# Kernel optimization log

Hardware: AMD Instinct MI355X
Metric: run time of the kernel (lower is better)

## Reference

```python
import jax, jax.numpy as jnp
import numpy as np
from jax import lax

EPS = 1e-5

def setup_inputs() -> dict:
    key = jax.random.key(0)
    ks = jax.random.split(key, 8)
    B, D, H, W = 2, 96, 96, 96
    K, N, R = 4, 16, 6
    return {
        "x": jax.random.normal(ks[0], (B, D, H, W), jnp.float32),
        "x_proj_weight": jax.random.normal(ks[1], (K, R + 2 * N, D), jnp.float32) * 0.05,
        "dt_projs_weight": jax.random.normal(ks[2], (K, D, R), jnp.float32) * 0.05,
        "dt_projs_bias": jax.random.normal(ks[3], (K, D), jnp.float32) * 0.05,
        "A_logs": jax.random.uniform(ks[4], (K * D, N), jnp.float32, 0.0, 1.0),
        "Ds": jax.random.normal(ks[5], (K * D,), jnp.float32) * 0.1,
        "norm_weight": jnp.ones((D,), jnp.float32),
        "norm_bias": jnp.zeros((D,), jnp.float32),
    }

def _cross_scan(x):
    # x: [B,C,H,W] -> xs: [B,4,C,L]; dirs: row-major, col-major, and their flips
    B, C, H, W = x.shape
    x_hw = x.reshape(B, C, H * W)
    x_wh = jnp.swapaxes(x, 2, 3).reshape(B, C, H * W)
    return jnp.stack([x_hw, x_wh, x_hw[..., ::-1], x_wh[..., ::-1]], axis=1)

def _cross_merge(ys, H, W):
    # ys: [B,4,C,L] -> y: [B,C,L]
    B, K, C, L = ys.shape
    ys = ys[:, 0:2] + ys[:, 2:4][..., ::-1]
    y_wh = jnp.swapaxes(ys[:, 1].reshape(B, C, W, H), 2, 3).reshape(B, C, L)
    return ys[:, 0] + y_wh

def _forward(x, x_proj_weight, dt_projs_weight, dt_projs_bias, A_logs, Ds,
             norm_weight, norm_bias):
    B, D, H, W = x.shape
    L = H * W
    K, _, R = dt_projs_weight.shape
    N = A_logs.shape[1]

    xs = _cross_scan(x)                                        # [B,K,D,L]
    x_dbl = jnp.einsum('bkdl,kcd->bkcl', xs, x_proj_weight)    # [B,K,R+2N,L]
    dts, Bs, Cs = x_dbl[:, :, :R], x_dbl[:, :, R:R + N], x_dbl[:, :, R + N:]
    dts = jnp.einsum('bkrl,kdr->bkdl', dts, dt_projs_weight)   # [B,K,D,L]

    A = -jnp.exp(A_logs).reshape(K, D, N)                      # [K,D,N]
    delta = jax.nn.softplus(dts + dt_projs_bias[None, :, :, None])  # [B,K,D,L]

    # time-major for scan
    u_t = jnp.moveaxis(xs, 3, 0)       # [L,B,K,D]
    d_t = jnp.moveaxis(delta, 3, 0)    # [L,B,K,D]
    B_t = jnp.moveaxis(Bs, 3, 0)       # [L,B,K,N]
    C_t = jnp.moveaxis(Cs, 3, 0)       # [L,B,K,N]

    def step(h, inp):
        u, dlt, b, c = inp
        h = jnp.exp(dlt[..., None] * A) * h + (dlt * u)[..., None] * b[:, :, None, :]
        y = jnp.einsum('bkdn,bkn->bkd', h, c)
        return h, y

    h0 = jnp.zeros((B, K, D, N), xs.dtype)
    _, ys = lax.scan(step, h0, (u_t, d_t, B_t, C_t))           # ys: [L,B,K,D]
    ys = jnp.moveaxis(ys, 0, 3)                                # [B,K,D,L]
    ys = ys + Ds.reshape(1, K, D, 1) * xs                      # skip term

    y = _cross_merge(ys, H, W)                                 # [B,D,L]
    y = jnp.swapaxes(y, 1, 2)                                  # [B,L,D]
    # out_norm: LayerNorm over channel dim
    mu = y.mean(-1, keepdims=True)
    var = y.var(-1, keepdims=True)
    y = (y - mu) / jnp.sqrt(var + EPS) * norm_weight + norm_bias
    return y.reshape(B, H, W, D)

def reference(x, x_proj_weight, dt_projs_weight, dt_projs_bias, A_logs, Ds,
              norm_weight, norm_bias):
    return _forward(x, x_proj_weight, dt_projs_weight, dt_projs_bias,
                    A_logs, Ds, norm_weight, norm_bias)
```

## Files before the change

kernel.cpp:

```cpp
#include <hip/hip_runtime.h>
#include <hip/hip_bf16.h>
#include <hip/hip_fp16.h>


constexpr int Bn = 2, Kn = 4, Dn = 96, Hn = 96, Wn = 96, Ln = Hn * Wn;
constexpr int Nn = 16, Rn = 6;
constexpr int CCn = 192, CLn = 48;

#define DI __device__ __forceinline__

DI float bf2f(unsigned short u) { return __uint_as_float(((unsigned)u) << 16); }
DI bool probe_bf16(const void* nw) { return ((const unsigned*)nw)[0] == 0x3F803F80u; }
DI float ld_in(const void* p, long i, bool bf) {
  return bf ? bf2f(((const unsigned short*)p)[i]) : ((const float*)p)[i];
}
DI float fexp2(float x) {
#if __has_builtin(__builtin_amdgcn_exp2f)
  return __builtin_amdgcn_exp2f(x);
#else
  return exp2f(x);
#endif
}
DI float softplus_fast(float v) {
  return (v > 15.f) ? v : __logf(1.f + __expf(v));
}
constexpr float LOG2E = 1.44269504088896340736f;

__global__ __launch_bounds__(256) void k_convert(
    const void* __restrict__ xpw, const void* __restrict__ dtw,
    const void* __restrict__ dtb, const void* __restrict__ Al,
    const void* __restrict__ Ds, const void* __restrict__ nw,
    const void* __restrict__ nb,
    float* __restrict__ wp_f, float* __restrict__ wdt_f,
    float* __restrict__ bias_f, float* __restrict__ Al_f,
    float* __restrict__ dsum, float* __restrict__ nw_f, float* __restrict__ nb_f) {
  bool bf = probe_bf16(nw);
  int gtid = blockIdx.x * 256 + threadIdx.x;
  int gs = gridDim.x * 256;
  for (int i = gtid; i < Kn * 38 * Dn; i += gs) wp_f[i] = ld_in(xpw, i, bf);
  for (int i = gtid; i < Kn * Dn * Rn; i += gs) wdt_f[i] = ld_in(dtw, i, bf);
  for (int i = gtid; i < Kn * Dn; i += gs) bias_f[i] = ld_in(dtb, i, bf);
  for (int i = gtid; i < Kn * Dn * Nn; i += gs)
    Al_f[i] = -__expf(ld_in(Al, i, bf)) * LOG2E;
  for (int i = gtid; i < Dn; i += gs) {
    dsum[i] = ld_in(Ds, i, bf) + ld_in(Ds, 96 + i, bf) +
              ld_in(Ds, 192 + i, bf) + ld_in(Ds, 288 + i, bf);
    nw_f[i] = ld_in(nw, i, bf);
    nb_f[i] = ld_in(nb, i, bf);
  }
}

__global__ __launch_bounds__(256) void k_prep(const void* __restrict__ x,
                                              const void* __restrict__ nwraw,
                                              float* __restrict__ xl,
                                              float* __restrict__ xlT) {
  __shared__ float tile[96 * 97];
  bool bf = probe_bf16(nwraw);
  int h = blockIdx.x, b = blockIdx.y;
  long srcbase = (long)b * Dn * Ln + (long)h * 96;
  for (int i = threadIdx.x; i < 96 * 96; i += 256) {
    int d = i / 96, w = i - d * 96;
    tile[d * 97 + w] = ld_in(x, srcbase + (long)d * Ln + w, bf);
  }
  __syncthreads();
  float* xlb = xl + (size_t)b * Ln * 96;
  float* xTb = xlT + (size_t)b * Ln * 96;
  for (int i = threadIdx.x; i < 96 * 96; i += 256) {
    int w = i / 96, d = i - w * 96;
    float v = tile[d * 97 + w];
    xlb[(size_t)(h * 96 + w) * 96 + d] = v;
    xTb[(size_t)(w * 96 + h) * 96 + d] = v;
  }
}

__global__ __launch_bounds__(256) void k_proj(
    const float* __restrict__ xl, const float* __restrict__ xlT,
    const float* __restrict__ wp_f, const float* __restrict__ wdt_f,
    const float* __restrict__ bias_f,
    __half2* __restrict__ ddu, __half* __restrict__ BCh) {
  constexpr int TL = 64;
  __shared__ __half xt[TL * 102];
  __shared__ float wp[40 * 100];
  __shared__ float xd[40 * 70];
  __shared__ float wdt[96 * 6];
  __shared__ float bias[96];
  int tile = blockIdx.x, k = blockIdx.y, b = blockIdx.z;
  int l0 = tile * TL;
  int tid = threadIdx.x;
  bool rev = (k & 2) != 0;

  for (int i = tid; i < 40 * 100; i += 256) {
    int c = i / 100, dd = i - c * 100;
    wp[i] = (c < 38 && dd < 96) ? wp_f[k * 38 * 96 + c * 96 + dd] : 0.f;
  }
  for (int i = tid; i < 96 * 6; i += 256) wdt[i] = wdt_f[k * 96 * 6 + i];
  if (tid < 96) bias[tid] = bias_f[k * 96 + tid];
  {
    const float* xsrc = ((k & 1) ? xlT : xl) + (size_t)b * Ln * 96;
    for (int i = tid; i < TL * 24; i += 256) {
      int r = i / 24, q = i - r * 24;
      int g = rev ? (Ln - 1 - l0 - r) : (l0 + r);
      float4 v = *(const float4*)(xsrc + (size_t)g * 96 + q * 4);
      *(__half2*)(&xt[r * 102 + q * 4]) = __floats2half2_rn(v.x, v.y);
      *(__half2*)(&xt[r * 102 + q * 4 + 2]) = __floats2half2_rn(v.z, v.w);
    }
  }
  __syncthreads();

  {
    int jg = tid & 31, cg = tid >> 5;
    int j0 = jg * 2, c0 = cg * 5;
    float acc[5][2];
#pragma unroll
    for (int i = 0; i < 5; ++i) { acc[i][0] = 0.f; acc[i][1] = 0.f; }
    for (int dd = 0; dd < 96; dd += 4) {
      float xv[2][4];
#pragma unroll
      for (int e = 0; e < 2; ++e) {
        float2 f01 = __half22float2(*(const __half2*)&xt[(j0 + e) * 102 + dd]);
        float2 f23 = __half22float2(*(const __half2*)&xt[(j0 + e) * 102 + dd + 2]);
        xv[e][0] = f01.x; xv[e][1] = f01.y; xv[e][2] = f23.x; xv[e][3] = f23.y;
      }
#pragma unroll
      for (int i = 0; i < 5; ++i) {
        float4 w4 = *(const float4*)(wp + (c0 + i) * 100 + dd);
        const float* w = (const float*)&w4;
#pragma unroll
        for (int q = 0; q < 4; ++q) {
          acc[i][0] = fmaf(xv[0][q], w[q], acc[i][0]);
          acc[i][1] = fmaf(xv[1][q], w[q], acc[i][1]);
        }
      }
    }
#pragma unroll
    for (int i = 0; i < 5; ++i)
      *(float2*)(xd + (c0 + i) * 70 + j0) = make_float2(acc[i][0], acc[i][1]);
  }
  __syncthreads();

  size_t bk = (size_t)b * 4 + k;
  {
    __half* o = BCh + (bk * (size_t)Ln + l0) * 32;
    for (int i = tid; i < TL * 32; i += 256) {
      int j = i >> 5, c = i & 31;
      o[i] = __float2half(xd[(6 + c) * 70 + j]);
    }
  }
  {
    int lp = tid >> 2, q = tid & 3, d0 = q * 24;
    float xr[6];
#pragma unroll
    for (int r = 0; r < 6; ++r) xr[r] = xd[r * 70 + lp];
    __half2* orow = ddu + (bk * (size_t)Ln + l0 + lp) * 96 + d0;
#pragma unroll
    for (int ii = 0; ii < 6; ++ii) {
      union { uint4 u4; __half2 h2[4]; } pk;
#pragma unroll
      for (int p = 0; p < 4; ++p) {
        int d = d0 + ii * 4 + p;
        float v = bias[d];
#pragma unroll
        for (int r = 0; r < 6; ++r) v = fmaf(xr[r], wdt[d * 6 + r], v);
        float sp = softplus_fast(v);
        float u = __half2float(xt[lp * 102 + d]);
        pk.h2[p] = __floats2half2_rn(sp, sp * u);
      }
      *(uint4*)(orow + ii * 4) = pk.u4;
    }
  }
}

__global__ __launch_bounds__(384) void k_scan1(
    const __half2* __restrict__ ddu, const __half* __restrict__ BCh,
    const float* __restrict__ Al_f, float* __restrict__ PSg) {
  __shared__ __half2 dd_s[CLn * 96];
  __shared__ __half b_s[CLn * 16];
  int chunk = blockIdx.x, k = blockIdx.y, b = blockIdx.z;
  int tid = threadIdx.x;
  int d = tid >> 2, ng = tid & 3, n0 = ng * 4;
  int bk = b * 4 + k;
  int bkd = bk * 96 + d;
  int t0 = chunk * CLn;
  float ac[4];
#pragma unroll
  for (int j = 0; j < 4; ++j) ac[j] = Al_f[(k * 96 + d) * 16 + n0 + j];
  {
    const uint4* dsrc = (const uint4*)(ddu + ((size_t)bk * Ln + t0) * 96);
    uint4* ddst = (uint4*)dd_s;
    for (int i = tid; i < CLn * 96 / 4; i += 384) ddst[i] = dsrc[i];
    const unsigned* bsrc = (const unsigned*)(BCh + ((size_t)bk * Ln + t0) * 32);
    unsigned* bdst = (unsigned*)b_s;
    for (int i = tid; i < CLn * 8; i += 384) {
      int t = i >> 3, q = i & 7;
      bdst[t * 8 + q] = bsrc[t * 16 + q];
    }
  }
  __syncthreads();

  float P[4] = {1.f, 1.f, 1.f, 1.f}, S[4] = {0.f, 0.f, 0.f, 0.f};
#pragma unroll 4
  for (int t = 0; t < CLn; ++t) {
    float2 f = __half22float2(dd_s[t * 96 + d]);
    union { uint2 u; __half2 h2[2]; } bv;
    bv.u = *(const uint2*)&b_s[t * 16 + n0];
    float2 b01 = __half22float2(bv.h2[0]);
    float2 b23 = __half22float2(bv.h2[1]);
    float Ba[4] = {b01.x, b01.y, b23.x, b23.y};
#pragma unroll
    for (int j = 0; j < 4; ++j) {
      float a = fexp2(f.x * ac[j]);
      P[j] *= a;
      S[j] = fmaf(a, S[j], f.y * Ba[j]);
    }
  }
  size_t ob = ((size_t)bkd * CCn + chunk) * 32 + n0;
  *(float4*)(PSg + ob) = make_float4(P[0], P[1], P[2], P[3]);
  *(float4*)(PSg + ob + 16) = make_float4(S[0], S[1], S[2], S[3]);
}

__global__ __launch_bounds__(256) void k_midscan(float* __restrict__ PSg) {
  __shared__ float Pl[256], Sl[256];
  int bkd = blockIdx.x;
  int tid = threadIdx.x;
  int g = tid >> 4, n = tid & 15;
  constexpr int CPG = CCn / 16;
  size_t base = ((size_t)bkd * CCn + (size_t)g * CPG) * 32 + n;
  float Pr[CPG], Sr[CPG];
#pragma unroll
  for (int i = 0; i < CPG; ++i) {
    Pr[i] = PSg[base + (size_t)i * 32];
    Sr[i] = PSg[base + (size_t)i * 32 + 16];
  }
  float Pa = 1.f, Sa = 0.f;
#pragma unroll
  for (int i = 0; i < CPG; ++i) { Sa = fmaf(Pr[i], Sa, Sr[i]); Pa *= Pr[i]; }
  Pl[tid] = Pa;
  Sl[tid] = Sa;
  __syncthreads();
#pragma unroll
  for (int s = 1; s < 16; s <<= 1) {
    float Pp = 1.f, Sp = 0.f;
    if (g >= s) { Pp = Pl[(g - s) * 16 + n]; Sp = Sl[(g - s) * 16 + n]; }
    __syncthreads();
    if (g >= s) {
      Sl[tid] = fmaf(Pl[tid], Sp, Sl[tid]);
      Pl[tid] *= Pp;
    }
    __syncthreads();
  }
  float h = (g == 0) ? 0.f : Sl[(g - 1) * 16 + n];
#pragma unroll
  for (int i = 0; i < CPG; ++i) {
    PSg[base + (size_t)i * 32] = h;
    h = fmaf(Pr[i], h, Sr[i]);
  }
}

__global__ __launch_bounds__(384) void k_scan2(
    const __half2* __restrict__ ddu, const __half* __restrict__ BCh,
    const float* __restrict__ Al_f, const float* __restrict__ PSg,
    __half* __restrict__ ysH) {
  __shared__ __half2 dd_s[CLn * 96];
  __shared__ __half bc_s[CLn * 32];
  int chunk = blockIdx.x, k = blockIdx.y, b = blockIdx.z;
  int tid = threadIdx.x;
  int d = tid >> 2, ng = tid & 3, n0 = ng * 4;
  int bk = b * 4 + k;
  int bkd = bk * 96 + d;
  int t0 = chunk * CLn;
  float ac[4];
#pragma unroll
  for (int j = 0; j < 4; ++j) ac[j] = Al_f[(k * 96 + d) * 16 + n0 + j];
  {
    const uint4* dsrc = (const uint4*)(ddu + ((size_t)bk * Ln + t0) * 96);
    uint4* ddst = (uint4*)dd_s;
    for (int i = tid; i < CLn * 96 / 4; i += 384) ddst[i] = dsrc[i];
    const uint4* bsrc = (const uint4*)(BCh + ((size_t)bk * Ln + t0) * 32);
    uint4* bdst = (uint4*)bc_s;
    for (int i = tid; i < CLn * 32 * 2 / 16; i += 384) bdst[i] = bsrc[i];
  }
  float4 h4 = *(const float4*)(PSg + ((size_t)bkd * CCn + chunk) * 32 + n0);
  float h[4] = {h4.x, h4.y, h4.z, h4.w};
  __syncthreads();

#pragma unroll 4
  for (int t = 0; t < CLn; ++t) {
    float2 f = __half22float2(dd_s[t * 96 + d]);
    union { uint2 u; __half2 h2[2]; } bv, cv;
    bv.u = *(const uint2*)&bc_s[t * 32 + n0];
    cv.u = *(const uint2*)&bc_s[t * 32 + 16 + n0];
    float2 b01 = __half22float2(bv.h2[0]);
    float2 b23 = __half22float2(bv.h2[1]);
    float2 c01 = __half22float2(cv.h2[0]);
    float2 c23 = __half22float2(cv.h2[1]);
    float Ba[4] = {b01.x, b01.y, b23.x, b23.y};
    float Ca[4] = {c01.x, c01.y, c23.x, c23.y};
    float py = 0.f;
#pragma unroll
    for (int j = 0; j < 4; ++j) {
      float a = fexp2(f.x * ac[j]);
      h[j] = fmaf(a, h[j], f.y * Ba[j]);
      py = fmaf(h[j], Ca[j], py);
    }
    py += __shfl_xor(py, 1);
    py += __shfl_xor(py, 2);
    if (ng == 0) ysH[((size_t)bk * Ln + t0 + t) * 96 + d] = __float2half(py);
  }
}

__global__ __launch_bounds__(256) void k_merge_ln(
    const __half* __restrict__ ysH, const float* __restrict__ xl,
    const float* __restrict__ dsum, const void* __restrict__ nwraw,
    const float* __restrict__ nw_f, const float* __restrict__ nb_f,
    void* __restrict__ outv) {
  __shared__ float yt[64 * 97];
  __shared__ float nwf[96], nbf[96], mu_s[64], rs_s[64];
  bool bf = probe_bf16(nwraw);
  int tile = blockIdx.x, b = blockIdx.y;
  int h0 = (tile / 12) * 8, w0 = (tile % 12) * 8;
  int tid = threadIdx.x;
  if (tid < 96) { nwf[tid] = nw_f[tid]; nbf[tid] = nb_f[tid]; }
  const __half* y0 = ysH + (size_t)(b * 4 + 0) * Ln * 96;
  const __half* y1 = ysH + (size_t)(b * 4 + 1) * Ln * 96;
  const __half* y2 = ysH + (size_t)(b * 4 + 2) * Ln * 96;
  const __half* y3 = ysH + (size_t)(b * 4 + 3) * Ln * 96;
  const float* xb = xl + (size_t)b * Ln * 96;
  for (int i = tid; i < 64 * 96; i += 256) {
    int rr = i / 96, d = i - rr * 96;
    int hh = h0 + (rr >> 3), ww = w0 + (rr & 7);
    int l = hh * 96 + ww, t1 = ww * 96 + hh;
    float v = __half2float(y0[(size_t)l * 96 + d]) +
              __half2float(y1[(size_t)t1 * 96 + d]) +
              __half2float(y2[(size_t)(Ln - 1 - l) * 96 + d]) +
              __half2float(y3[(size_t)(Ln - 1 - t1) * 96 + d]) +
              dsum[d] * xb[(size_t)l * 96 + d];
    yt[rr * 97 + d] = v;
  }
  __syncthreads();
  if (tid < 64) {
    float s = 0.f, ss = 0.f;
#pragma unroll 4
    for (int d = 0; d < 96; ++d) {
      float v = yt[tid * 97 + d];
      s += v;
      ss += v * v;
    }
    float mu = s * (1.f / 96.f);
    float var = fmaxf(ss * (1.f / 96.f) - mu * mu, 0.f);
    mu_s[tid] = mu;
    rs_s[tid] = rsqrtf(var + 1e-5f);
  }
  __syncthreads();
  for (int i = tid; i < 64 * 96; i += 256) {
    int rr = i / 96, d = i - rr * 96;
    int hh = h0 + (rr >> 3), ww = w0 + (rr & 7);
    size_t idx = ((size_t)b * Ln + hh * 96 + ww) * 96 + d;
    float v = (yt[rr * 97 + d] - mu_s[rr]) * rs_s[rr] * nwf[d] + nbf[d];
    if (bf) ((__hip_bfloat16*)outv)[idx] = __float2bfloat16(v);
    else    ((float*)outv)[idx] = v;
  }
}

extern "C" void kernel_launch(void* const* d_in, const int* in_sizes, int n_in,
                              void* d_out, int out_size, void* d_ws, size_t ws_size,
                              hipStream_t stream) {
  const void* x   = d_in[0];
  const void* xpw = d_in[1];
  const void* dtw = d_in[2];
  const void* dtb = d_in[3];
  const void* Al  = d_in[4];
  const void* Ds  = d_in[5];
  const void* nw  = d_in[6];
  const void* nb  = d_in[7];

  char* ws = (char*)d_ws;
  size_t off = 0;
  auto alloc = [&](size_t bytes) {
    char* p = ws + off;
    off += (bytes + 511) & ~(size_t)511;
    return p;
  };
  float* xl    = (float*)alloc((size_t)Bn * Ln * Dn * 4);
  float* xlT   = (float*)alloc((size_t)Bn * Ln * Dn * 4);
  float* wp_f  = (float*)alloc((size_t)Kn * 38 * Dn * 4);
  float* wdt_f = (float*)alloc((size_t)Kn * Dn * Rn * 4);
  float* bias_f= (float*)alloc((size_t)Kn * Dn * 4);
  float* Al_f  = (float*)alloc((size_t)Kn * Dn * Nn * 4);
  float* dsum  = (float*)alloc((size_t)Dn * 4);
  float* nw_f  = (float*)alloc((size_t)Dn * 4);
  float* nb_f  = (float*)alloc((size_t)Dn * 4);
  __half2* ddu = (__half2*)alloc((size_t)Bn * Kn * Ln * Dn * 4);
  __half* BCh  = (__half*)alloc((size_t)Bn * Kn * Ln * 32 * 2);
  float* PS    = (float*)alloc((size_t)Bn * Kn * Dn * CCn * 32 * 4);
  __half* ysH  = (__half*)alloc((size_t)Bn * Kn * Ln * Dn * 2);
  (void)ws_size; (void)in_sizes; (void)n_in; (void)out_size;

  k_convert<<<dim3(64), dim3(256), 0, stream>>>(xpw, dtw, dtb, Al, Ds, nw, nb,
                                                wp_f, wdt_f, bias_f, Al_f,
                                                dsum, nw_f, nb_f);
  k_prep<<<dim3(Hn, Bn), dim3(256), 0, stream>>>(x, nw, xl, xlT);
  k_proj<<<dim3(Ln / 64, Kn, Bn), dim3(256), 0, stream>>>(xl, xlT, wp_f, wdt_f,
                                                          bias_f, ddu, BCh);
  k_scan1<<<dim3(CCn, Kn, Bn), dim3(384), 0, stream>>>(ddu, BCh, Al_f, PS);
  k_midscan<<<dim3(Bn * Kn * Dn), dim3(256), 0, stream>>>(PS);
  k_scan2<<<dim3(CCn, Kn, Bn), dim3(384), 0, stream>>>(ddu, BCh, Al_f, PS, ysH);
  k_merge_ln<<<dim3(144, Bn), dim3(256), 0, stream>>>(ysH, xl, dsum, nw, nw_f,
                                                      nb_f, d_out);
}
```

Measured before the change: 203.7 us.

## Fuse projection with first scan pass and merge weight conversion into prep

Merges the weight-conversion kernel into the transpose/prep kernel, and fuses the x-projection kernel with the first chunked-scan pass so each block computes projections for a 64-step chunk and scans it straight from shared memory. This removes two launches and the global re-read of ddu/BC in scan1. The chunk count changes from 192x48 to 144x64, which alters the parallelism of the scan passes. The block grows to 384 threads with a third of them idle during the projection GEMM, and shared memory use per block rises.

```diff
diff --git a/kernel.cpp b/kernel.cpp
--- a/kernel.cpp
+++ b/kernel.cpp
@@ -5,7 +5,7 @@
 
 constexpr int Bn = 2, Kn = 4, Dn = 96, Hn = 96, Wn = 96, Ln = Hn * Wn;
 constexpr int Nn = 16, Rn = 6;
-constexpr int CCn = 192, CLn = 48;
+constexpr int CCn = 144, CLn = 64;
 
 #define DI __device__ __forceinline__
 
@@ -26,46 +26,41 @@
 }
 constexpr float LOG2E = 1.44269504088896340736f;
 
-__global__ __launch_bounds__(256) void k_convert(
-    const void* __restrict__ xpw, const void* __restrict__ dtw,
-    const void* __restrict__ dtb, const void* __restrict__ Al,
-    const void* __restrict__ Ds, const void* __restrict__ nw,
-    const void* __restrict__ nb,
+__global__ __launch_bounds__(256) void k_prep(
+    const void* __restrict__ x, const void* __restrict__ xpw,
+    const void* __restrict__ dtw, const void* __restrict__ dtb,
+    const void* __restrict__ Al, const void* __restrict__ Ds,
+    const void* __restrict__ nw, const void* __restrict__ nb,
+    float* __restrict__ xl, float* __restrict__ xlT,
     float* __restrict__ wp_f, float* __restrict__ wdt_f,
     float* __restrict__ bias_f, float* __restrict__ Al_f,
     float* __restrict__ dsum, float* __restrict__ nw_f, float* __restrict__ nb_f) {
+  __shared__ float tile[96 * 97];
   bool bf = probe_bf16(nw);
-  int gtid = blockIdx.x * 256 + threadIdx.x;
-  int gs = gridDim.x * 256;
-  for (int i = gtid; i < Kn * 38 * Dn; i += gs) wp_f[i] = ld_in(xpw, i, bf);
-  for (int i = gtid; i < Kn * Dn * Rn; i += gs) wdt_f[i] = ld_in(dtw, i, bf);
-  for (int i = gtid; i < Kn * Dn; i += gs) bias_f[i] = ld_in(dtb, i, bf);
-  for (int i = gtid; i < Kn * Dn * Nn; i += gs)
+  int h = blockIdx.x, b = blockIdx.y;
+  int tid = threadIdx.x;
+  int fi = (blockIdx.y * gridDim.x + blockIdx.x) * 256 + tid;
+  int fgs = gridDim.x * gridDim.y * 256;
+  for (int i = fi; i < Kn * 38 * Dn; i += fgs) wp_f[i] = ld_in(xpw, i, bf);
+  for (int i = fi; i < Kn * Dn * Rn; i += fgs) wdt_f[i] = ld_in(dtw, i, bf);
+  for (int i = fi; i < Kn * Dn; i += fgs) bias_f[i] = ld_in(dtb, i, bf);
+  for (int i = fi; i < Kn * Dn * Nn; i += fgs)
     Al_f[i] = -__expf(ld_in(Al, i, bf)) * LOG2E;
-  for (int i = gtid; i < Dn; i += gs) {
+  for (int i = fi; i < Dn; i += fgs) {
     dsum[i] = ld_in(Ds, i, bf) + ld_in(Ds, 96 + i, bf) +
               ld_in(Ds, 192 + i, bf) + ld_in(Ds, 288 + i, bf);
     nw_f[i] = ld_in(nw, i, bf);
     nb_f[i] = ld_in(nb, i, bf);
   }
-}
-
-__global__ __launch_bounds__(256) void k_prep(const void* __restrict__ x,
-                                              const void* __restrict__ nwraw,
-                                              float* __restrict__ xl,
-                                              float* __restrict__ xlT) {
-  __shared__ float tile[96 * 97];
-  bool bf = probe_bf16(nwraw);
-  int h = blockIdx.x, b = blockIdx.y;
   long srcbase = (long)b * Dn * Ln + (long)h * 96;
-  for (int i = threadIdx.x; i < 96 * 96; i += 256) {
+  for (int i = tid; i < 96 * 96; i += 256) {
     int d = i / 96, w = i - d * 96;
     tile[d * 97 + w] = ld_in(x, srcbase + (long)d * Ln + w, bf);
   }
   __syncthreads();
   float* xlb = xl + (size_t)b * Ln * 96;
   float* xTb = xlT + (size_t)b * Ln * 96;
-  for (int i = threadIdx.x; i < 96 * 96; i += 256) {
+  for (int i = tid; i < 96 * 96; i += 256) {
     int w = i / 96, d = i - w * 96;
     float v = tile[d * 97 + w];
     xlb[(size_t)(h * 96 + w) * 96 + d] = v;
@@ -73,31 +68,33 @@
   }
 }
 
-__global__ __launch_bounds__(256) void k_proj(
+__global__ __launch_bounds__(384) void k_projscan(
     const float* __restrict__ xl, const float* __restrict__ xlT,
     const float* __restrict__ wp_f, const float* __restrict__ wdt_f,
-    const float* __restrict__ bias_f,
-    __half2* __restrict__ ddu, __half* __restrict__ BCh) {
-  constexpr int TL = 64;
-  __shared__ __half xt[TL * 102];
+    const float* __restrict__ bias_f, const float* __restrict__ Al_f,
+    __half2* __restrict__ ddu, __half* __restrict__ BCh,
+    float* __restrict__ PSg) {
+  constexpr int TL = CLn;
   __shared__ float wp[40 * 100];
   __shared__ float xd[40 * 70];
+  __shared__ __half xt[TL * 102];
+  __shared__ __half2 dd_s[TL * 96];
   __shared__ float wdt[96 * 6];
   __shared__ float bias[96];
-  int tile = blockIdx.x, k = blockIdx.y, b = blockIdx.z;
-  int l0 = tile * TL;
+  int chunk = blockIdx.x, k = blockIdx.y, b = blockIdx.z;
+  int l0 = chunk * TL;
   int tid = threadIdx.x;
   bool rev = (k & 2) != 0;
 
-  for (int i = tid; i < 40 * 100; i += 256) {
+  for (int i = tid; i < 40 * 100; i += 384) {
     int c = i / 100, dd = i - c * 100;
     wp[i] = (c < 38 && dd < 96) ? wp_f[k * 38 * 96 + c * 96 + dd] : 0.f;
   }
-  for (int i = tid; i < 96 * 6; i += 256) wdt[i] = wdt_f[k * 96 * 6 + i];
+  for (int i = tid; i < 96 * 6; i += 384) wdt[i] = wdt_f[k * 96 * 6 + i];
   if (tid < 96) bias[tid] = bias_f[k * 96 + tid];
   {
     const float* xsrc = ((k & 1) ? xlT : xl) + (size_t)b * Ln * 96;
-    for (int i = tid; i < TL * 24; i += 256) {
+    for (int i = tid; i < TL * 24; i += 384) {
       int r = i / 24, q = i - r * 24;
       int g = rev ? (Ln - 1 - l0 - r) : (l0 + r);
       float4 v = *(const float4*)(xsrc + (size_t)g * 96 + q * 4);
@@ -107,7 +104,7 @@
   }
   __syncthreads();
 
-  {
+  if (tid < 256) {
     int jg = tid & 31, cg = tid >> 5;
     int j0 = jg * 2, c0 = cg * 5;
     float acc[5][2];
@@ -141,19 +138,20 @@
   size_t bk = (size_t)b * 4 + k;
   {
     __half* o = BCh + (bk * (size_t)Ln + l0) * 32;
-    for (int i = tid; i < TL * 32; i += 256) {
+    for (int i = tid; i < TL * 32; i += 384) {
       int j = i >> 5, c = i & 31;
       o[i] = __float2half(xd[(6 + c) * 70 + j]);
     }
   }
   {
-    int lp = tid >> 2, q = tid & 3, d0 = q * 24;
+    int lp = tid / 6, q = tid - lp * 6;
+    int d0 = q * 16;
     float xr[6];
 #pragma unroll
     for (int r = 0; r < 6; ++r) xr[r] = xd[r * 70 + lp];
     __half2* orow = ddu + (bk * (size_t)Ln + l0 + lp) * 96 + d0;
 #pragma unroll
-    for (int ii = 0; ii < 6; ++ii) {
+    for (int ii = 0; ii < 4; ++ii) {
       union { uint4 u4; __half2 h2[4]; } pk;
 #pragma unroll
       for (int p = 0; p < 4; ++p) {
@@ -166,56 +164,35 @@
         pk.h2[p] = __floats2half2_rn(sp, sp * u);
       }
       *(uint4*)(orow + ii * 4) = pk.u4;
-    }
-  }
-}
-
-__global__ __launch_bounds__(384) void k_scan1(
-    const __half2* __restrict__ ddu, const __half* __restrict__ BCh,
-    const float* __restrict__ Al_f, float* __restrict__ PSg) {
-  __shared__ __half2 dd_s[CLn * 96];
-  __shared__ __half b_s[CLn * 16];
-  int chunk = blockIdx.x, k = blockIdx.y, b = blockIdx.z;
-  int tid = threadIdx.x;
-  int d = tid >> 2, ng = tid & 3, n0 = ng * 4;
-  int bk = b * 4 + k;
-  int bkd = bk * 96 + d;
-  int t0 = chunk * CLn;
-  float ac[4];
-#pragma unroll
-  for (int j = 0; j < 4; ++j) ac[j] = Al_f[(k * 96 + d) * 16 + n0 + j];
-  {
-    const uint4* dsrc = (const uint4*)(ddu + ((size_t)bk * Ln + t0) * 96);
-    uint4* ddst = (uint4*)dd_s;
-    for (int i = tid; i < CLn * 96 / 4; i += 384) ddst[i] = dsrc[i];
-    const unsigned* bsrc = (const unsigned*)(BCh + ((size_t)bk * Ln + t0) * 32);
-    unsigned* bdst = (unsigned*)b_s;
-    for (int i = tid; i < CLn * 8; i += 384) {
-      int t = i >> 3, q = i & 7;
-      bdst[t * 8 + q] = bsrc[t * 16 + q];
-    }
-  }
-  __syncthreads();
-
-  float P[4] = {1.f, 1.f, 1.f, 1.f}, S[4] = {0.f, 0.f, 0.f, 0.f};
+      *(uint4*)(&dd_s[lp * 96 + d0 + ii * 4]) = pk.u4;
+    }
+  }
+  __syncthreads();
+
+  {
+    int d = tid >> 2, ng = tid & 3, n0 = ng * 4;
+    int bkd = (int)bk * 96 + d;
+    float ac[4];
+#pragma unroll
+    for (int j = 0; j < 4; ++j) ac[j] = Al_f[(k * 96 + d) * 16 + n0 + j];
+    float P[4] = {1.f, 1.f, 1.f, 1.f}, S[4] = {0.f, 0.f, 0.f, 0.f};
 #pragma unroll 4
-  for (int t = 0; t < CLn; ++t) {
-    float2 f = __half22float2(dd_s[t * 96 + d]);
-    union { uint2 u; __half2 h2[2]; } bv;
-    bv.u = *(const uint2*)&b_s[t * 16 + n0];
-    float2 b01 = __half22float2(bv.h2[0]);
-    float2 b23 = __half22float2(bv.h2[1]);
-    float Ba[4] = {b01.x, b01.y, b23.x, b23.y};
-#pragma unroll
-    for (int j = 0; j < 4; ++j) {
-      float a = fexp2(f.x * ac[j]);
-      P[j] *= a;
-      S[j] = fmaf(a, S[j], f.y * Ba[j]);
-    }
-  }
-  size_t ob = ((size_t)bkd * CCn + chunk) * 32 + n0;
-  *(float4*)(PSg + ob) = make_float4(P[0], P[1], P[2], P[3]);
-  *(float4*)(PSg + ob + 16) = make_float4(S[0], S[1], S[2], S[3]);
+    for (int t = 0; t < TL; ++t) {
+      float2 f = __half22float2(dd_s[t * 96 + d]);
+      float Ba[4];
+#pragma unroll
+      for (int j = 0; j < 4; ++j) Ba[j] = xd[(6 + n0 + j) * 70 + t];
+#pragma unroll
+      for (int j = 0; j < 4; ++j) {
+        float a = fexp2(f.x * ac[j]);
+        P[j] *= a;
+        S[j] = fmaf(a, S[j], f.y * Ba[j]);
+      }
+    }
+    size_t ob = ((size_t)bkd * CCn + chunk) * 32 + n0;
+    *(float4*)(PSg + ob) = make_float4(P[0], P[1], P[2], P[3]);
+    *(float4*)(PSg + ob + 16) = make_float4(S[0], S[1], S[2], S[3]);
+  }
 }
 
 __global__ __launch_bounds__(256) void k_midscan(float* __restrict__ PSg) {
@@ -395,13 +372,11 @@
   __half* ysH  = (__half*)alloc((size_t)Bn * Kn * Ln * Dn * 2);
   (void)ws_size; (void)in_sizes; (void)n_in; (void)out_size;
 
-  k_convert<<<dim3(64), dim3(256), 0, stream>>>(xpw, dtw, dtb, Al, Ds, nw, nb,
-                                                wp_f, wdt_f, bias_f, Al_f,
-                                                dsum, nw_f, nb_f);
-  k_prep<<<dim3(Hn, Bn), dim3(256), 0, stream>>>(x, nw, xl, xlT);
-  k_proj<<<dim3(Ln / 64, Kn, Bn), dim3(256), 0, stream>>>(xl, xlT, wp_f, wdt_f,
-                                                          bias_f, ddu, BCh);
-  k_scan1<<<dim3(CCn, Kn, Bn), dim3(384), 0, stream>>>(ddu, BCh, Al_f, PS);
+  k_prep<<<dim3(Hn, Bn), dim3(256), 0, stream>>>(
+      x, xpw, dtw, dtb, Al, Ds, nw, nb, xl, xlT, wp_f, wdt_f, bias_f, Al_f,
+      dsum, nw_f, nb_f);
+  k_projscan<<<dim3(CCn, Kn, Bn), dim3(384), 0, stream>>>(
+      xl, xlT, wp_f, wdt_f, bias_f, Al_f, ddu, BCh, PS);
   k_midscan<<<dim3(Bn * Kn * Dn), dim3(256), 0, stream>>>(PS);
   k_scan2<<<dim3(CCn, Kn, Bn), dim3(384), 0, stream>>>(ddu, BCh, Al_f, PS, ysH);
   k_merge_ln<<<dim3(144, Bn), dim3(256), 0, stream>>>(ysH, xl, dsum, nw, nw_f,
```

Result: slower. 216.7 us (+6.4%).

## Fuse weight conversion into transpose prep kernel and retune scan chunking

Applied to the files above, without the earlier changes.

Merges the parameter conversion kernel into the input transpose kernel, so the conversion loops run grid-stride across the prep grid, removing one launch. Also changes scan chunking from 192 chunks of length 48 to 144 chunks of length 64, which gives fewer blocks with longer sequential work and a smaller partial-state buffer for the mid-scan. The chunk change moves the balance between parallelism and carry-propagation work.

```diff
diff --git a/kernel.cpp b/kernel.cpp
--- a/kernel.cpp
+++ b/kernel.cpp
@@ -5,7 +5,7 @@
 
 constexpr int Bn = 2, Kn = 4, Dn = 96, Hn = 96, Wn = 96, Ln = Hn * Wn;
 constexpr int Nn = 16, Rn = 6;
-constexpr int CCn = 192, CLn = 48;
+constexpr int CCn = 144, CLn = 64;
 
 #define DI __device__ __forceinline__
 
@@ -26,46 +26,41 @@
 }
 constexpr float LOG2E = 1.44269504088896340736f;
 
-__global__ __launch_bounds__(256) void k_convert(
-    const void* __restrict__ xpw, const void* __restrict__ dtw,
-    const void* __restrict__ dtb, const void* __restrict__ Al,
-    const void* __restrict__ Ds, const void* __restrict__ nw,
-    const void* __restrict__ nb,
+__global__ __launch_bounds__(256) void k_prep(
+    const void* __restrict__ x, const void* __restrict__ xpw,
+    const void* __restrict__ dtw, const void* __restrict__ dtb,
+    const void* __restrict__ Al, const void* __restrict__ Ds,
+    const void* __restrict__ nw, const void* __restrict__ nb,
+    float* __restrict__ xl, float* __restrict__ xlT,
     float* __restrict__ wp_f, float* __restrict__ wdt_f,
     float* __restrict__ bias_f, float* __restrict__ Al_f,
     float* __restrict__ dsum, float* __restrict__ nw_f, float* __restrict__ nb_f) {
+  __shared__ float tile[96 * 97];
   bool bf = probe_bf16(nw);
-  int gtid = blockIdx.x * 256 + threadIdx.x;
-  int gs = gridDim.x * 256;
-  for (int i = gtid; i < Kn * 38 * Dn; i += gs) wp_f[i] = ld_in(xpw, i, bf);
-  for (int i = gtid; i < Kn * Dn * Rn; i += gs) wdt_f[i] = ld_in(dtw, i, bf);
-  for (int i = gtid; i < Kn * Dn; i += gs) bias_f[i] = ld_in(dtb, i, bf);
-  for (int i = gtid; i < Kn * Dn * Nn; i += gs)
+  int h = blockIdx.x, b = blockIdx.y;
+  int tid = threadIdx.x;
+  int fi = (blockIdx.y * gridDim.x + blockIdx.x) * 256 + tid;
+  int fgs = gridDim.x * gridDim.y * 256;
+  for (int i = fi; i < Kn * 38 * Dn; i += fgs) wp_f[i] = ld_in(xpw, i, bf);
+  for (int i = fi; i < Kn * Dn * Rn; i += fgs) wdt_f[i] = ld_in(dtw, i, bf);
+  for (int i = fi; i < Kn * Dn; i += fgs) bias_f[i] = ld_in(dtb, i, bf);
+  for (int i = fi; i < Kn * Dn * Nn; i += fgs)
     Al_f[i] = -__expf(ld_in(Al, i, bf)) * LOG2E;
-  for (int i = gtid; i < Dn; i += gs) {
+  for (int i = fi; i < Dn; i += fgs) {
     dsum[i] = ld_in(Ds, i, bf) + ld_in(Ds, 96 + i, bf) +
               ld_in(Ds, 192 + i, bf) + ld_in(Ds, 288 + i, bf);
     nw_f[i] = ld_in(nw, i, bf);
     nb_f[i] = ld_in(nb, i, bf);
   }
-}
-
-__global__ __launch_bounds__(256) void k_prep(const void* __restrict__ x,
-                                              const void* __restrict__ nwraw,
-                                              float* __restrict__ xl,
-                                              float* __restrict__ xlT) {
-  __shared__ float tile[96 * 97];
-  bool bf = probe_bf16(nwraw);
-  int h = blockIdx.x, b = blockIdx.y;
   long srcbase = (long)b * Dn * Ln + (long)h * 96;
-  for (int i = threadIdx.x; i < 96 * 96; i += 256) {
+  for (int i = tid; i < 96 * 96; i += 256) {
     int d = i / 96, w = i - d * 96;
     tile[d * 97 + w] = ld_in(x, srcbase + (long)d * Ln + w, bf);
   }
   __syncthreads();
   float* xlb = xl + (size_t)b * Ln * 96;
   float* xTb = xlT + (size_t)b * Ln * 96;
-  for (int i = threadIdx.x; i < 96 * 96; i += 256) {
+  for (int i = tid; i < 96 * 96; i += 256) {
     int w = i / 96, d = i - w * 96;
     float v = tile[d * 97 + w];
     xlb[(size_t)(h * 96 + w) * 96 + d] = v;
@@ -395,10 +390,9 @@
   __half* ysH  = (__half*)alloc((size_t)Bn * Kn * Ln * Dn * 2);
   (void)ws_size; (void)in_sizes; (void)n_in; (void)out_size;
 
-  k_convert<<<dim3(64), dim3(256), 0, stream>>>(xpw, dtw, dtb, Al, Ds, nw, nb,
-                                                wp_f, wdt_f, bias_f, Al_f,
-                                                dsum, nw_f, nb_f);
-  k_prep<<<dim3(Hn, Bn), dim3(256), 0, stream>>>(x, nw, xl, xlT);
+  k_prep<<<dim3(Hn, Bn), dim3(256), 0, stream>>>(
+      x, xpw, dtw, dtb, Al, Ds, nw, nb, xl, xlT, wp_f, wdt_f, bias_f, Al_f,
+      dsum, nw_f, nb_f);
   k_proj<<<dim3(Ln / 64, Kn, Bn), dim3(256), 0, stream>>>(xl, xlT, wp_f, wdt_f,
                                                           bias_f, ddu, BCh);
   k_scan1<<<dim3(CCn, Kn, Bn), dim3(384), 0, stream>>>(ddu, BCh, Al_f, PS);
```

Result: no change. 205.3 us (+0.8%).
